# Optimization experiments

Measured on AMD Instinct MI355X. Metric: run time of the kernel, lower is better.

## Reference

```python
import jax, jax.numpy as jnp
import numpy as np

B, H, S, DK, DV = 2, 16, 2048, 64, 64


def setup_inputs() -> dict:
    key = jax.random.key(0)
    kq, kk, kv = jax.random.split(key, 3)
    Q = jax.random.normal(kq, (B, H, S, DK), dtype=jnp.float32)
    K = jax.random.normal(kk, (B, H, S, DK), dtype=jnp.float32)
    V = jax.random.normal(kv, (B, H, S, DV), dtype=jnp.float32)
    # causal mask: True = masked (upper triangle), broadcast to [B,H,S,S]
    causal = jnp.triu(jnp.ones((S, S), dtype=bool), k=1)
    attn_mask = jnp.broadcast_to(causal, (B, H, S, S))
    return {"Q": Q, "K": K, "V": V, "attn_mask": attn_mask}


def reference(Q, K, V, attn_mask):
    d_k = Q.shape[-1]
    # scores: [B,H,len_q,len_k]
    scores = jnp.einsum('bhqd,bhkd->bhqk', Q, K) / jnp.sqrt(jnp.float32(d_k))
    scores = jnp.where(attn_mask, -jnp.inf, scores)
    attn = jax.nn.softmax(scores, axis=-1)
    # context: [B,H,len_q,d_v]
    context = jnp.einsum('bhqk,bhkv->bhqv', attn, V)
    return context
```

## Files before the change

kernel.cpp:

```cpp
#include <hip/hip_runtime.h>
#include <hip/hip_bf16.h>
#include <math.h>

#define S_LEN 2048
#define DKV 64
#define NBH 32
#define QBLK 128
#define NQB (S_LEN / QBLK)
#define NKT (S_LEN / 64)
#define TILE_SH 4096

typedef __attribute__((ext_vector_type(8))) short bf16x8;
typedef __attribute__((ext_vector_type(16))) float f32x16;
typedef __attribute__((ext_vector_type(4))) float f32x4;
typedef __attribute__((ext_vector_type(4))) unsigned uint4v;

__device__ __forceinline__ short f2bf(float f) {
    union { float f; unsigned u; } x; x.f = f;
    unsigned r = (x.u + 0x7FFFu + ((x.u >> 16) & 1u)) >> 16;
    return (short)r;
}

__device__ __forceinline__ unsigned cvtpk(float lo, float hi) {
    unsigned r;
    asm("v_cvt_pk_bf16_f32 %0, %1, %2" : "=v"(r) : "v"(lo), "v"(hi));
    return r;
}

__global__ __launch_bounds__(256)
void prep_kv(const float* __restrict__ K, const float* __restrict__ V,
             short* __restrict__ wsK, short* __restrict__ wsV) {
    const int tile = blockIdx.x, bh = blockIdx.y, tid = threadIdx.x;
    const float* Kp = K + ((size_t)bh * S_LEN + tile * 64) * DKV;
    const float* Vp = V + ((size_t)bh * S_LEN + tile * 64) * DKV;
    short* outK = wsK + ((size_t)bh * NKT + tile) * TILE_SH;
    short* outV = wsV + ((size_t)bh * NKT + tile) * TILE_SH;

    __shared__ short Vl[64 * 64];

#pragma unroll
    for (int i = 0; i < 2; ++i) {
        const int chunk = i * 256 + tid;
        const int row = chunk >> 3, c8 = chunk & 7;
        const float* ks = Kp + row * DKV + c8 * 8;
        float4 a = *(const float4*)ks, b = *(const float4*)(ks + 4);
        bf16x8 t;
        t[0] = f2bf(a.x); t[1] = f2bf(a.y); t[2] = f2bf(a.z); t[3] = f2bf(a.w);
        t[4] = f2bf(b.x); t[5] = f2bf(b.y); t[6] = f2bf(b.z); t[7] = f2bf(b.w);
        const int sidxK = (((c8 >> 1) * 2 + (row >> 5)) * 64) |
                          (((c8 & 1) << 5) | (row & 31));
        *(bf16x8*)(outK + sidxK * 8) = t;

        const float* vs = Vp + row * DKV + c8 * 8;
        float4 c = *(const float4*)vs, d = *(const float4*)(vs + 4);
        bf16x8 u;
        u[0] = f2bf(c.x); u[1] = f2bf(c.y); u[2] = f2bf(c.z); u[3] = f2bf(c.w);
        u[4] = f2bf(d.x); u[5] = f2bf(d.y); u[6] = f2bf(d.z); u[7] = f2bf(d.w);
        *(bf16x8*)&Vl[chunk * 8] = u;
    }
    __syncthreads();
#pragma unroll
    for (int i = 0; i < 2; ++i) {
        const int chunk = i * 256 + tid;
        const int vd = chunk >> 3, k8 = chunk & 7;
        bf16x8 t;
#pragma unroll
        for (int j = 0; j < 8; ++j) t[j] = Vl[(k8 * 8 + j) * 64 + vd];
        const int sidxV = (((k8 >> 1) * 2 + (vd >> 5)) * 64) |
                          (((k8 & 1) << 5) | (vd & 31));
        *(bf16x8*)(outV + sidxV * 8) = t;
    }
}

__global__ __launch_bounds__(256, 2)
void attn_fwd(const float* __restrict__ Q, const short* __restrict__ wsK,
              const short* __restrict__ wsV, float* __restrict__ O) {
    const int tid = threadIdx.x;
    const int l   = tid & 63;
    const int w   = tid >> 6;
    const int qc  = w & 1;
    const int ks  = w >> 1;
    const int h   = l >> 5;
    const int q31 = l & 31;

    const int id  = blockIdx.x;
    const int bh  = ((id & 7) << 2) | ((id >> 3) & 3);
    const int r5  = (id >> 5) & 7;
    const int qb  = (id < 256) ? (15 - r5) : r5;

    __shared__ float comb[2][2][64][34];

    const float SCALE = 0.125f * 1.4426950408889634f;

    bf16x8 qf[2][4];
#pragma unroll
    for (int sp = 0; sp < 2; ++sp) {
        const int qrow = qb * QBLK + qc * 64 + sp * 32 + q31;
        const float* qr = Q + ((size_t)bh * S_LEN + qrow) * DKV;
#pragma unroll
        for (int c = 0; c < 4; ++c) {
            const int k0 = c * 16 + h * 8;
            float4 f0 = *(const float4*)(qr + k0);
            float4 f1 = *(const float4*)(qr + k0 + 4);
            bf16x8 t;
            t[0] = f2bf(f0.x * SCALE); t[1] = f2bf(f0.y * SCALE);
            t[2] = f2bf(f0.z * SCALE); t[3] = f2bf(f0.w * SCALE);
            t[4] = f2bf(f1.x * SCALE); t[5] = f2bf(f1.y * SCALE);
            t[6] = f2bf(f1.z * SCALE); t[7] = f2bf(f1.w * SCALE);
            qf[sp][c] = t;
        }
    }

    const char* gK = (const char*)(wsK + (size_t)bh * NKT * TILE_SH);
    const char* gV = (const char*)(wsV + (size_t)bh * NKT * TILE_SH);
    const int lb = l * 16;

    float m[2] = {-3.0e38f, -3.0e38f}, lsum[2] = {0.0f, 0.0f};
    f32x16 oacc[2][2];
#pragma unroll
    for (int sp = 0; sp < 2; ++sp)
#pragma unroll
        for (int vh = 0; vh < 2; ++vh)
#pragma unroll
            for (int r = 0; r < 16; ++r) oacc[sp][vh][r] = 0.0f;

    const int tmax = 2 * qb + qc;
    for (int t = ks; t <= tmax; t += 2) {
        const char* kT = gK + (size_t)t * (TILE_SH * 2);
        const char* vT = gV + (size_t)t * (TILE_SH * 2);

        bf16x8 kf[8], vf[8];
#pragma unroll
        for (int i = 0; i < 8; ++i) kf[i] = *(const bf16x8*)(kT + i * 1024 + lb);
#pragma unroll
        for (int i = 0; i < 8; ++i) vf[i] = *(const bf16x8*)(vT + i * 1024 + lb);

#pragma unroll
        for (int sp = 0; sp < 2; ++sp) {
            const int qrow = qb * QBLK + qc * 64 + sp * 32 + q31;

            f32x16 sacc[2];
#pragma unroll
            for (int th = 0; th < 2; ++th)
#pragma unroll
                for (int r = 0; r < 16; ++r) sacc[th][r] = 0.0f;

            __builtin_amdgcn_s_setprio(1);
#pragma unroll
            for (int c = 0; c < 4; ++c)
#pragma unroll
                for (int th = 0; th < 2; ++th)
                    sacc[th] = __builtin_amdgcn_mfma_f32_32x32x16_bf16(
                        kf[c * 2 + th], qf[sp][c], sacc[th], 0, 0, 0);
            __builtin_amdgcn_s_setprio(0);

            if (t == tmax) {
                const int kv0 = t * 64;
#pragma unroll
                for (int th = 0; th < 2; ++th)
#pragma unroll
                    for (int r = 0; r < 16; ++r) {
                        const int key_g = kv0 + 32 * th + (r & 3) + 8 * (r >> 2) + 4 * h;
                        if (key_g > qrow) sacc[th][r] = -3.0e38f;
                    }
            }

            float t16[16];
#pragma unroll
            for (int r = 0; r < 16; ++r) t16[r] = fmaxf(sacc[0][r], sacc[1][r]);
#pragma unroll
            for (int r = 0; r < 8; ++r) t16[r] = fmaxf(t16[r], t16[r + 8]);
#pragma unroll
            for (int r = 0; r < 4; ++r) t16[r] = fmaxf(t16[r], t16[r + 4]);
            float mx = fmaxf(fmaxf(t16[0], t16[1]), fmaxf(t16[2], t16[3]));
            mx = fmaxf(mx, __shfl_xor(mx, 32));

            const bool skip = __all(mx <= m[sp] + 8.0f);
            if (!skip) {
                const float mn = fmaxf(m[sp], mx);
                const float sfv = __builtin_amdgcn_exp2f(m[sp] - mn);
                m[sp] = mn;
                lsum[sp] *= sfv;
#pragma unroll
                for (int vh = 0; vh < 2; ++vh)
#pragma unroll
                    for (int r = 0; r < 16; ++r) oacc[sp][vh][r] *= sfv;
            }

            float rs = 0.0f;
            __builtin_amdgcn_s_setprio(1);
#pragma unroll
            for (int c = 0; c < 4; ++c) {
                const int th = c >> 1, cc = c & 1;
                float p8[8];
#pragma unroll
                for (int j = 0; j < 8; ++j) {
                    p8[j] = __builtin_amdgcn_exp2f(sacc[th][8 * cc + j] - m[sp]);
                    rs += p8[j];
                }
                const unsigned W00 = cvtpk(p8[0], p8[1]);
                const unsigned W01 = cvtpk(p8[2], p8[3]);
                const unsigned W10 = cvtpk(p8[4], p8[5]);
                const unsigned W11 = cvtpk(p8[6], p8[7]);
                const unsigned S0 = h ? W00 : W10;
                const unsigned S1 = h ? W01 : W11;
                const unsigned K0 = h ? W10 : W00;
                const unsigned K1 = h ? W11 : W01;
                const unsigned Y0 = __shfl_xor(S0, 32);
                const unsigned Y1 = __shfl_xor(S1, 32);
                uint4v pwv;
                pwv[0] = h ? Y0 : K0;
                pwv[1] = h ? Y1 : K1;
                pwv[2] = h ? K0 : Y0;
                pwv[3] = h ? K1 : Y1;
                const bf16x8 pa = __builtin_bit_cast(bf16x8, pwv);
#pragma unroll
                for (int vh = 0; vh < 2; ++vh)
                    oacc[sp][vh] = __builtin_amdgcn_mfma_f32_32x32x16_bf16(
                        vf[c * 2 + vh], pa, oacc[sp][vh], 0, 0, 0);
            }
            __builtin_amdgcn_s_setprio(0);

            rs += __shfl_xor(rs, 32);
            lsum[sp] += rs;
        }
    }

    if (ks == 1) {
#pragma unroll
        for (int sp = 0; sp < 2; ++sp) {
            float* cp = &comb[qc][sp][l][0];
            cp[0] = m[sp]; cp[1] = lsum[sp];
#pragma unroll
            for (int vh = 0; vh < 2; ++vh)
#pragma unroll
                for (int r = 0; r < 16; ++r) cp[2 + vh * 16 + r] = oacc[sp][vh][r];
        }
    }
    __syncthreads();
    if (ks == 0) {
#pragma unroll
        for (int sp = 0; sp < 2; ++sp) {
            const float* cp = &comb[qc][sp][l][0];
            const float m1 = cp[0], l1 = cp[1];
            const float ms = fmaxf(m[sp], m1);
            const float f0 = __builtin_amdgcn_exp2f(m[sp] - ms);
            const float f1 = __builtin_amdgcn_exp2f(m1 - ms);
            const float inv = 1.0f / (lsum[sp] * f0 + l1 * f1);
            const int qrow = qb * QBLK + qc * 64 + sp * 32 + q31;
            float* Op = O + ((size_t)bh * S_LEN + qrow) * DKV;
#pragma unroll
            for (int vh = 0; vh < 2; ++vh) {
#pragma unroll
                for (int g2 = 0; g2 < 4; ++g2) {
                    f32x4 ov;
#pragma unroll
                    for (int d = 0; d < 4; ++d)
                        ov[d] = (oacc[sp][vh][4 * g2 + d] * f0 +
                                 cp[2 + vh * 16 + 4 * g2 + d] * f1) * inv;
                    *(f32x4*)(Op + 32 * vh + 8 * g2 + 4 * h) = ov;
                }
            }
        }
    }
}

extern "C" void kernel_launch(void* const* d_in, const int* in_sizes, int n_in,
                              void* d_out, int out_size, void* d_ws, size_t ws_size,
                              hipStream_t stream) {
    const float* Q = (const float*)d_in[0];
    const float* K = (const float*)d_in[1];
    const float* V = (const float*)d_in[2];
    float* O = (float*)d_out;

    short* wsK = (short*)d_ws;
    short* wsV = wsK + (size_t)NBH * NKT * TILE_SH;

    dim3 gridp(NKT, NBH);
    prep_kv<<<gridp, 256, 0, stream>>>(K, V, wsK, wsV);
    attn_fwd<<<dim3(NQB * NBH), 256, 0, stream>>>(Q, wsK, wsV, O);
}
```

Measured before the change: 52.44 us.

## Double-buffer K tiles through LDS with async global_load_lds prefetch

Each wave now streams its K tiles into a per-wave double buffer in LDS using global_load_lds, prefetching tile t+2 while tile t is being computed. The combine scratch aliases the same 64KB shared array. The goal is to hide K load latency behind the MFMA work. In exchange, LDS use per block rises to 64KB, which may cap occupancy, and the s_waitcnt vmcnt(0) at the top of each iteration also waits on the V loads, which limits how much overlap is gained.

```diff
diff --git a/kernel.cpp b/kernel.cpp
--- a/kernel.cpp
+++ b/kernel.cpp
@@ -26,6 +26,11 @@
     asm("v_cvt_pk_bf16_f32 %0, %1, %2" : "=v"(r) : "v"(lo), "v"(hi));
     return r;
 }
+
+#define GLOAD_LDS16(g, s)                                                        \
+    __builtin_amdgcn_global_load_lds(                                            \
+        (const __attribute__((address_space(1))) unsigned*)(g),                  \
+        (__attribute__((address_space(3))) unsigned*)(s), 16, 0, 0)
 
 __global__ __launch_bounds__(256)
 void prep_kv(const float* __restrict__ K, const float* __restrict__ V,
@@ -88,7 +93,9 @@
     const int r5  = (id >> 5) & 7;
     const int qb  = (id < 256) ? (15 - r5) : r5;
 
-    __shared__ float comb[2][2][64][34];
+    __shared__ char smem[65536];
+    char* kstaW = smem + w * 16384;
+    float* combp = (float*)smem;
 
     const float SCALE = 0.125f * 1.4426950408889634f;
 
@@ -125,13 +132,32 @@
             for (int r = 0; r < 16; ++r) oacc[sp][vh][r] = 0.0f;
 
     const int tmax = 2 * qb + qc;
+
+    if (ks <= tmax) {
+        const char* kT = gK + (size_t)ks * (TILE_SH * 2);
+#pragma unroll
+        for (int i = 0; i < 8; ++i)
+            GLOAD_LDS16(kT + i * 1024 + lb, kstaW + i * 1024);
+    }
+
+    int cur = 0;
     for (int t = ks; t <= tmax; t += 2) {
-        const char* kT = gK + (size_t)t * (TILE_SH * 2);
+        asm volatile("s_waitcnt vmcnt(0)" ::: "memory");
+        bf16x8 kf[8];
+#pragma unroll
+        for (int i = 0; i < 8; ++i)
+            kf[i] = *(const bf16x8*)(kstaW + cur * 8192 + i * 1024 + lb);
+
+        if (t + 2 <= tmax) {
+            const char* kT2 = gK + (size_t)(t + 2) * (TILE_SH * 2);
+            char* nb = kstaW + (cur ^ 1) * 8192;
+#pragma unroll
+            for (int i = 0; i < 8; ++i)
+                GLOAD_LDS16(kT2 + i * 1024 + lb, nb + i * 1024);
+        }
+
         const char* vT = gV + (size_t)t * (TILE_SH * 2);
-
-        bf16x8 kf[8], vf[8];
-#pragma unroll
-        for (int i = 0; i < 8; ++i) kf[i] = *(const bf16x8*)(kT + i * 1024 + lb);
+        bf16x8 vf[8];
 #pragma unroll
         for (int i = 0; i < 8; ++i) vf[i] = *(const bf16x8*)(vT + i * 1024 + lb);
 
@@ -224,12 +250,14 @@
             rs += __shfl_xor(rs, 32);
             lsum[sp] += rs;
         }
-    }
-
+        cur ^= 1;
+    }
+
+    __syncthreads();
     if (ks == 1) {
 #pragma unroll
         for (int sp = 0; sp < 2; ++sp) {
-            float* cp = &comb[qc][sp][l][0];
+            float* cp = combp + ((qc * 2 + sp) * 64 + l) * 34;
             cp[0] = m[sp]; cp[1] = lsum[sp];
 #pragma unroll
             for (int vh = 0; vh < 2; ++vh)
@@ -241,7 +269,7 @@
     if (ks == 0) {
 #pragma unroll
         for (int sp = 0; sp < 2; ++sp) {
-            const float* cp = &comb[qc][sp][l][0];
+            const float* cp = combp + ((qc * 2 + sp) * 64 + l) * 34;
             const float m1 = cp[0], l1 = cp[1];
             const float ms = fmaxf(m[sp], m1);
             const float f0 = __builtin_amdgcn_exp2f(m[sp] - ms);
```

Result: no change. 52.03 us (-0.8%).
